# Optimization experiments

Hardware: AMD Instinct MI355X
Metric: run time of the kernel (lower is better)

## Reference

```python
import jax, jax.numpy as jnp
import numpy as np

B, H, T, K = 4, 32, 2048, 64
V = K


def setup_inputs() -> dict:
    key = jax.random.key(0)
    k1, k2, k3, k4, k5 = jax.random.split(key, 5)
    r = jax.random.normal(k1, (B, H, T, K), dtype=jnp.float32)
    k = jax.random.normal(k2, (B, H, T, K), dtype=jnp.float32)
    v = jax.random.normal(k3, (B, H, T, V), dtype=jnp.float32)
    # w is a log-decay; keep it negative so exp(w) in (0,1) and the T-step
    # recurrence is stable (matches real RWKV-6 decay values)
    w = -2.0 * jax.random.uniform(k4, (B, H, T, K), dtype=jnp.float32)
    u = jax.random.normal(k5, (H, K), dtype=jnp.float32)
    initial_state = jnp.zeros((B, H, K, V), dtype=jnp.float32)
    return {"r": r, "k": k, "v": v, "w": w, "u": u, "initial_state": initial_state}


def _rwkv6_scan(r, k, v, w, u, initial_state):
    scale = 1.0
    q = r * scale
    decay = jnp.exp(w)  # [B,H,T,K], matches torch: b_w = exp(w)

    # time-major for scan: [T,B,H,K]
    qT = jnp.moveaxis(q, 2, 0)
    kT = jnp.moveaxis(k, 2, 0)
    vT = jnp.moveaxis(v, 2, 0)
    wT = jnp.moveaxis(decay, 2, 0)

    u_b = u[None, :, :, None]  # [1,H,K,1] broadcast like torch b_u

    def step(h, inp):
        bq, bk, bv, bw = inp  # each [B,H,K] (bv is [B,H,V])
        kv = bk[..., :, None] * bv[..., None, :]          # [B,H,K,V]
        o = jnp.einsum('bhkv,bhk->bhv', h + kv * u_b, bq)  # sum over K
        h = h * bw[..., None] + kv                         # decay-gated update
        return h, o

    final_state, oT = jax.lax.scan(step, initial_state, (qT, kT, vT, wT))
    o = jnp.moveaxis(oT, 0, 2)  # [B,H,T,V]
    return o, final_state


def reference(r, k, v, w, u, initial_state):
    return _rwkv6_scan(r, k, v, w, u, initial_state)
```

## Files before the change

kernel.cpp:

```cpp
#include <hip/hip_runtime.h>
#include <math.h>


#define Bdim 4
#define Hdim 32
#define Tdim 2048
#define Kdim 64
#define Vdim 64
#define NC   32
#define CL   64
#define LP   72

typedef __attribute__((ext_vector_type(8))) short short8;
typedef __attribute__((ext_vector_type(4))) float float4_;

__device__ __forceinline__ short f2bf(float x) {
    unsigned u = __float_as_uint(x);
    unsigned r = (u + 0x7FFFu + ((u >> 16) & 1u)) >> 16;
    return (short)r;
}

#define MFMA(a, b, c) __builtin_amdgcn_mfma_f32_16x16x32_bf16(a, b, c, 0, 0, 0)

__global__ __launch_bounds__(512) void rwkv6_fused(
    const float* __restrict__ rin, const float* __restrict__ kin,
    const float* __restrict__ vin, const float* __restrict__ win,
    const float* __restrict__ uin, const float* __restrict__ init,
    float* __restrict__ oout, float* __restrict__ fin)
{
    __shared__ __attribute__((aligned(16))) short Qh[CL * LP];
    __shared__ __attribute__((aligned(16))) short Kh[CL * LP];
    __shared__ __attribute__((aligned(16))) short Qt[CL * LP];
    __shared__ __attribute__((aligned(16))) short Am[CL * LP];
    __shared__ __attribute__((aligned(16))) short Vt[32 * LP];
    __shared__ __attribute__((aligned(16))) short Ht[32 * LP];
    __shared__ float bsum[8 * 64];
    __shared__ float Dd[CL];

    const int tid  = threadIdx.x;
    const int wv   = tid >> 6;
    const int lane = tid & 63;
    const int quad = lane >> 4, r = lane & 15;

    const int bid = blockIdx.x;
    const int vh  = bid >> 7;
    const int bh  = bid & 127;
    const int h_idx = bh & (Hdim - 1);

    const int m_s = wv >> 2;
    const int n_s = wv & 3;
    const int k_  = 16 * n_s + r;
    const int i_o = wv >> 1;
    const int n_o = wv & 1;

    const float u_ = uin[h_idx * Kdim + lane];

    for (int i = tid; i < CL * LP; i += 512) Am[i] = 0;

    float h[4];
#pragma unroll
    for (int reg = 0; reg < 4; ++reg) {
        const int vloc = 16 * m_s + quad * 4 + reg;
        h[reg] = init[((size_t)bh * Kdim + k_) * Vdim + 32 * vh + vloc];
        Ht[vloc * LP + k_] = f2bf(h[reg]);
    }

    const int tv = tid >> 3;
    const int vl = (tid & 7) * 4;

    float wl[8], ql[8], kl[8];
    float4_ vl4;
    {
        const size_t b0 = (size_t)bh * Tdim * Kdim;
#pragma unroll
        for (int tt = 0; tt < 8; ++tt) {
            const int t = 8 * wv + tt;
            wl[tt] = win[b0 + t * Kdim + lane];
            ql[tt] = rin[b0 + t * Kdim + lane];
            kl[tt] = kin[b0 + t * Kdim + lane];
        }
        vl4 = *(const float4_*)&vin[b0 + tv * Kdim + 32 * vh + vl];
    }

    auto atile = [&](int i, int j) {
        const int trow = 16 * i + r;
        short8 qa0 = *(const short8*)&Qh[trow * LP + quad * 8];
        short8 qa1 = *(const short8*)&Qh[trow * LP + 32 + quad * 8];
        const int srow = 16 * j + r;
        const int sb = (srow >> 3) & 7;
        short8 kb0 = *(const short8*)&Kh[srow * LP + ((quad ^ sb) << 3)];
        short8 kb1 = *(const short8*)&Kh[srow * LP + (((quad + 4) ^ sb) << 3)];
        float4_ acc = {0.f, 0.f, 0.f, 0.f};
        acc = MFMA(qa0, kb0, acc);
        acc = MFMA(qa1, kb1, acc);
#pragma unroll
        for (int reg = 0; reg < 4; ++reg) {
            const int tg = 16 * i + quad * 4 + reg;
            const float val = (tg > srow) ? acc[reg] : ((tg == srow) ? Dd[tg] : 0.f);
            Am[tg * LP + srow] = f2bf(val);
        }
    };

    for (int c = 0; c < NC; ++c) {
        const size_t base = ((size_t)bh * Tdim + (size_t)c * CL) * Kdim;

        float wreg[8];
        float cwl = 0.f;
#pragma unroll
        for (int tt = 0; tt < 8; ++tt) { wreg[tt] = wl[tt]; cwl += wl[tt]; }
        bsum[wv * 64 + lane] = cwl;
#pragma unroll
        for (int i = 0; i < 4; ++i) Vt[(vl + i) * LP + tv] = f2bf(vl4[i]);
        __syncthreads();

        float b[8];
#pragma unroll
        for (int j = 0; j < 8; ++j) b[j] = bsum[j * 64 + lane];
        float pref = 0.f;
#pragma unroll
        for (int j = 0; j < 8; ++j) if (j < wv) pref += b[j];
        const float Cmid = b[0] + b[1] + b[2] + b[3];
        const float eC = __expf(Cmid);
        float cwrun = pref;
#pragma unroll
        for (int tt = 0; tt < 8; ++tt) {
            const int t = 8 * wv + tt;
            const float cwp = cwrun;
            cwrun += wreg[tt];
            const float e1 = __expf(cwp - Cmid);
            Qh[t * LP + lane] = f2bf(ql[tt] * e1);
            Qt[t * LP + lane] = f2bf(ql[tt] * e1 * eC);
            const float e2 = __expf(Cmid - cwrun);
            Kh[t * LP + ((((lane >> 3) ^ ((t >> 3) & 7)) << 3) | (lane & 7))]
                = f2bf(kl[tt] * e2);
            float d3 = ql[tt] * u_ * kl[tt];
#pragma unroll
            for (int off = 32; off > 0; off >>= 1) d3 += __shfl_xor(d3, off);
            if (lane == 0) Dd[t] = d3;
        }
        if (c + 1 < NC) {
            const size_t nb = base + (size_t)CL * Kdim;
#pragma unroll
            for (int tt = 0; tt < 8; ++tt) {
                const int t = 8 * wv + tt;
                wl[tt] = win[nb + t * Kdim + lane];
                ql[tt] = rin[nb + t * Kdim + lane];
                kl[tt] = kin[nb + t * Kdim + lane];
            }
            vl4 = *(const float4_*)&vin[nb + tv * Kdim + 32 * vh + vl];
        }
        __syncthreads();

        {
            int i0, j0;
            if (wv == 0)      { i0 = 0; j0 = 0; }
            else if (wv < 3)  { i0 = 1; j0 = wv - 1; }
            else if (wv < 6)  { i0 = 2; j0 = wv - 3; }
            else              { i0 = 3; j0 = wv - 6; }
            atile(i0, j0);
            if (wv < 2) atile(3, 2 + wv);
        }
        __syncthreads();

        {
            const int trow = 16 * i_o + r;
            short8 aa0 = *(const short8*)&Am[trow * LP + quad * 8];
            short8 aa1 = *(const short8*)&Am[trow * LP + 32 + quad * 8];
            short8 qt0 = *(const short8*)&Qt[trow * LP + quad * 8];
            short8 qt1 = *(const short8*)&Qt[trow * LP + 32 + quad * 8];
            const int vrow = 16 * n_o + r;
            short8 vb0 = *(const short8*)&Vt[vrow * LP + quad * 8];
            short8 vb1 = *(const short8*)&Vt[vrow * LP + 32 + quad * 8];
            short8 hb0 = *(const short8*)&Ht[vrow * LP + quad * 8];
            short8 hb1 = *(const short8*)&Ht[vrow * LP + 32 + quad * 8];
            float4_ o4 = {0.f, 0.f, 0.f, 0.f};
            o4 = MFMA(aa0, vb0, o4);
            o4 = MFMA(aa1, vb1, o4);
            o4 = MFMA(qt0, hb0, o4);
            o4 = MFMA(qt1, hb1, o4);
            float* op = oout + base;
#pragma unroll
            for (int reg = 0; reg < 4; ++reg)
                op[(16 * i_o + quad * 4 + reg) * Vdim + 32 * vh + 16 * n_o + r] = o4[reg];
        }

        float4_ sc = {0.f, 0.f, 0.f, 0.f};
        {
            const int vrow = 16 * m_s + r;
            short8 va0 = *(const short8*)&Vt[vrow * LP + quad * 8];
            short8 va1 = *(const short8*)&Vt[vrow * LP + 32 + quad * 8];
            short8 kc0, kc1;
            const int kb8 = k_ >> 3, k7 = k_ & 7;
#pragma unroll
            for (int j2 = 0; j2 < 8; ++j2) {
                const int s0 = quad * 8 + j2;
                kc0[j2] = Kh[s0 * LP + ((((kb8 ^ (s0 >> 3)) & 7) << 3) | k7)];
                const int s1 = 32 + s0;
                kc1[j2] = Kh[s1 * LP + ((((kb8 ^ (s1 >> 3)) & 7) << 3) | k7)];
            }
            sc = MFMA(va0, kc0, sc);
            sc = MFMA(va1, kc1, sc);
        }
        float totk = 0.f, cmk = 0.f;
#pragma unroll
        for (int j = 0; j < 8; ++j) {
            const float bb = bsum[j * 64 + k_];
            totk += bb;
            if (j < 4) cmk += bb;
        }
        __syncthreads();

        {
            const float eA = __expf(totk);
            const float eS = __expf(totk - cmk);
#pragma unroll
            for (int reg = 0; reg < 4; ++reg) {
                h[reg] = h[reg] * eA + sc[reg] * eS;
                Ht[(16 * m_s + quad * 4 + reg) * LP + k_] = f2bf(h[reg]);
            }
        }
    }

#pragma unroll
    for (int reg = 0; reg < 4; ++reg)
        fin[((size_t)bh * Kdim + k_) * Vdim + 32 * vh + 16 * m_s + quad * 4 + reg] = h[reg];
}

extern "C" void kernel_launch(void* const* d_in, const int* in_sizes, int n_in,
                              void* d_out, int out_size, void* d_ws, size_t ws_size,
                              hipStream_t stream) {
    const float* r    = (const float*)d_in[0];
    const float* k    = (const float*)d_in[1];
    const float* v    = (const float*)d_in[2];
    const float* w    = (const float*)d_in[3];
    const float* u    = (const float*)d_in[4];
    const float* init = (const float*)d_in[5];

    float* o   = (float*)d_out;
    float* fin = o + (size_t)Bdim * Hdim * Tdim * Vdim;

    (void)d_ws; (void)ws_size;
    rwkv6_fused<<<Bdim * Hdim * 2, 512, 0, stream>>>(r, k, v, w, u, init, o, fin);
}
```

Baseline: 311.3 us.

## Add transposed K buffer, swizzled V/H LDS layouts, and lightweight barriers

Adds a transposed copy of the scaled K chunk (KhT) written as packed 16-byte rows, so the state-update MFMA operand becomes two vector LDS reads instead of sixteen scalar gathers. Vt and Ht move to an XOR-swizzled block layout, V is loaded with a different thread mapping and written as packed 4-element stores, and global loads are regrouped by tensor. The __syncthreads calls are replaced by a custom barrier that waits only on LDS counters, so outstanding global prefetches are not drained at each barrier. The cost is extra LDS capacity and stores for the KhT copy, plus reliance on the hand-written barrier being sufficient.

New measurement: 303.5 us. 2.5% less time.

```diff
diff --git a/kernel.cpp b/kernel.cpp
--- a/kernel.cpp
+++ b/kernel.cpp
@@ -12,6 +12,7 @@
 #define LP   72
 
 typedef __attribute__((ext_vector_type(8))) short short8;
+typedef __attribute__((ext_vector_type(4))) short short4_;
 typedef __attribute__((ext_vector_type(4))) float float4_;
 
 __device__ __forceinline__ short f2bf(float x) {
@@ -21,6 +22,13 @@
 }
 
 #define MFMA(a, b, c) __builtin_amdgcn_mfma_f32_16x16x32_bf16(a, b, c, 0, 0, 0)
+
+__device__ __forceinline__ void wg_barrier() {
+    __builtin_amdgcn_sched_barrier(0);
+    asm volatile("s_waitcnt lgkmcnt(0)");
+    __builtin_amdgcn_s_barrier();
+    __builtin_amdgcn_sched_barrier(0);
+}
 
 __global__ __launch_bounds__(512) void rwkv6_fused(
     const float* __restrict__ rin, const float* __restrict__ kin,
@@ -30,6 +38,7 @@
 {
     __shared__ __attribute__((aligned(16))) short Qh[CL * LP];
     __shared__ __attribute__((aligned(16))) short Kh[CL * LP];
+    __shared__ __attribute__((aligned(16))) short KhT[CL * LP];
     __shared__ __attribute__((aligned(16))) short Qt[CL * LP];
     __shared__ __attribute__((aligned(16))) short Am[CL * LP];
     __shared__ __attribute__((aligned(16))) short Vt[32 * LP];
@@ -55,6 +64,14 @@
 
     const float u_ = uin[h_idx * Kdim + lane];
 
+    const int svrow = tid & 31;
+    const int skq   = tid >> 5;
+
+    auto blk_addr = [](const short* buf, int row, int blk) -> const char* {
+        const int phys = blk ^ ((row >> 3) & 3);
+        return (const char*)buf + row * 144 + phys * 16;
+    };
+
     for (int i = tid; i < CL * LP; i += 512) Am[i] = 0;
 
     float h[4];
@@ -62,24 +79,22 @@
     for (int reg = 0; reg < 4; ++reg) {
         const int vloc = 16 * m_s + quad * 4 + reg;
         h[reg] = init[((size_t)bh * Kdim + k_) * Vdim + 32 * vh + vloc];
-        Ht[vloc * LP + k_] = f2bf(h[reg]);
+        const int hb = ((k_ >> 3) ^ ((vloc >> 3) & 3));
+        *(short*)((char*)Ht + vloc * 144 + hb * 16 + (k_ & 7) * 2) = f2bf(h[reg]);
     }
 
-    const int tv = tid >> 3;
-    const int vl = (tid & 7) * 4;
-
-    float wl[8], ql[8], kl[8];
-    float4_ vl4;
+    float wl[8], ql[8], kl[8], vls[4];
     {
         const size_t b0 = (size_t)bh * Tdim * Kdim;
 #pragma unroll
-        for (int tt = 0; tt < 8; ++tt) {
-            const int t = 8 * wv + tt;
-            wl[tt] = win[b0 + t * Kdim + lane];
-            ql[tt] = rin[b0 + t * Kdim + lane];
-            kl[tt] = kin[b0 + t * Kdim + lane];
-        }
-        vl4 = *(const float4_*)&vin[b0 + tv * Kdim + 32 * vh + vl];
+        for (int tt = 0; tt < 8; ++tt) wl[tt] = win[b0 + (8 * wv + tt) * Kdim + lane];
+#pragma unroll
+        for (int i = 0; i < 4; ++i)
+            vls[i] = vin[b0 + (4 * skq + i) * Kdim + 32 * vh + svrow];
+#pragma unroll
+        for (int tt = 0; tt < 8; ++tt) ql[tt] = rin[b0 + (8 * wv + tt) * Kdim + lane];
+#pragma unroll
+        for (int tt = 0; tt < 8; ++tt) kl[tt] = kin[b0 + (8 * wv + tt) * Kdim + lane];
     }
 
     auto atile = [&](int i, int j) {
@@ -109,9 +124,14 @@
 #pragma unroll
         for (int tt = 0; tt < 8; ++tt) { wreg[tt] = wl[tt]; cwl += wl[tt]; }
         bsum[wv * 64 + lane] = cwl;
-#pragma unroll
-        for (int i = 0; i < 4; ++i) Vt[(vl + i) * LP + tv] = f2bf(vl4[i]);
-        __syncthreads();
+        {
+            short4_ pack;
+#pragma unroll
+            for (int i = 0; i < 4; ++i) pack[i] = f2bf(vls[i]);
+            const int vb = ((skq >> 1) ^ ((svrow >> 3) & 3));
+            *(short4_*)((char*)Vt + svrow * 144 + vb * 16 + (skq & 1) * 8) = pack;
+        }
+        wg_barrier();
 
         float b[8];
 #pragma unroll
@@ -122,6 +142,7 @@
         const float Cmid = b[0] + b[1] + b[2] + b[3];
         const float eC = __expf(Cmid);
         float cwrun = pref;
+        short8 khrow;
 #pragma unroll
         for (int tt = 0; tt < 8; ++tt) {
             const int t = 8 * wv + tt;
@@ -131,25 +152,31 @@
             Qh[t * LP + lane] = f2bf(ql[tt] * e1);
             Qt[t * LP + lane] = f2bf(ql[tt] * e1 * eC);
             const float e2 = __expf(Cmid - cwrun);
-            Kh[t * LP + ((((lane >> 3) ^ ((t >> 3) & 7)) << 3) | (lane & 7))]
-                = f2bf(kl[tt] * e2);
+            const short kv = f2bf(kl[tt] * e2);
+            Kh[t * LP + ((((lane >> 3) ^ ((t >> 3) & 7)) << 3) | (lane & 7))] = kv;
+            khrow[tt] = kv;
             float d3 = ql[tt] * u_ * kl[tt];
 #pragma unroll
             for (int off = 32; off > 0; off >>= 1) d3 += __shfl_xor(d3, off);
             if (lane == 0) Dd[t] = d3;
         }
+        {
+            const int kb = (wv ^ ((lane >> 3) & 3));
+            *(short8*)((char*)KhT + lane * 144 + kb * 16) = khrow;
+        }
         if (c + 1 < NC) {
             const size_t nb = base + (size_t)CL * Kdim;
 #pragma unroll
-            for (int tt = 0; tt < 8; ++tt) {
-                const int t = 8 * wv + tt;
-                wl[tt] = win[nb + t * Kdim + lane];
-                ql[tt] = rin[nb + t * Kdim + lane];
-                kl[tt] = kin[nb + t * Kdim + lane];
-            }
-            vl4 = *(const float4_*)&vin[nb + tv * Kdim + 32 * vh + vl];
-        }
-        __syncthreads();
+            for (int tt = 0; tt < 8; ++tt) wl[tt] = win[nb + (8 * wv + tt) * Kdim + lane];
+#pragma unroll
+            for (int i = 0; i < 4; ++i)
+                vls[i] = vin[nb + (4 * skq + i) * Kdim + 32 * vh + svrow];
+#pragma unroll
+            for (int tt = 0; tt < 8; ++tt) ql[tt] = rin[nb + (8 * wv + tt) * Kdim + lane];
+#pragma unroll
+            for (int tt = 0; tt < 8; ++tt) kl[tt] = kin[nb + (8 * wv + tt) * Kdim + lane];
+        }
+        wg_barrier();
 
         {
             int i0, j0;
@@ -160,7 +187,7 @@
             atile(i0, j0);
             if (wv < 2) atile(3, 2 + wv);
         }
-        __syncthreads();
+        wg_barrier();
 
         {
             const int trow = 16 * i_o + r;
@@ -169,10 +196,10 @@
             short8 qt0 = *(const short8*)&Qt[trow * LP + quad * 8];
             short8 qt1 = *(const short8*)&Qt[trow * LP + 32 + quad * 8];
             const int vrow = 16 * n_o + r;
-            short8 vb0 = *(const short8*)&Vt[vrow * LP + quad * 8];
-            short8 vb1 = *(const short8*)&Vt[vrow * LP + 32 + quad * 8];
-            short8 hb0 = *(const short8*)&Ht[vrow * LP + quad * 8];
-            short8 hb1 = *(const short8*)&Ht[vrow * LP + 32 + quad * 8];
+            short8 vb0 = *(const short8*)blk_addr(Vt, vrow, quad);
+            short8 vb1 = *(const short8*)blk_addr(Vt, vrow, quad + 4);
+            short8 hb0 = *(const short8*)blk_addr(Ht, vrow, quad);
+            short8 hb1 = *(const short8*)blk_addr(Ht, vrow, quad + 4);
             float4_ o4 = {0.f, 0.f, 0.f, 0.f};
             o4 = MFMA(aa0, vb0, o4);
             o4 = MFMA(aa1, vb1, o4);
@@ -187,17 +214,10 @@
         float4_ sc = {0.f, 0.f, 0.f, 0.f};
         {
             const int vrow = 16 * m_s + r;
-            short8 va0 = *(const short8*)&Vt[vrow * LP + quad * 8];
-            short8 va1 = *(const short8*)&Vt[vrow * LP + 32 + quad * 8];
-            short8 kc0, kc1;
-            const int kb8 = k_ >> 3, k7 = k_ & 7;
-#pragma unroll
-            for (int j2 = 0; j2 < 8; ++j2) {
-                const int s0 = quad * 8 + j2;
-                kc0[j2] = Kh[s0 * LP + ((((kb8 ^ (s0 >> 3)) & 7) << 3) | k7)];
-                const int s1 = 32 + s0;
-                kc1[j2] = Kh[s1 * LP + ((((kb8 ^ (s1 >> 3)) & 7) << 3) | k7)];
-            }
+            short8 va0 = *(const short8*)blk_addr(Vt, vrow, quad);
+            short8 va1 = *(const short8*)blk_addr(Vt, vrow, quad + 4);
+            short8 kc0 = *(const short8*)blk_addr(KhT, k_, quad);
+            short8 kc1 = *(const short8*)blk_addr(KhT, k_, quad + 4);
             sc = MFMA(va0, kc0, sc);
             sc = MFMA(va1, kc1, sc);
         }
@@ -208,7 +228,7 @@
             totk += bb;
             if (j < 4) cmk += bb;
         }
-        __syncthreads();
+        wg_barrier();
 
         {
             const float eA = __expf(totk);
@@ -216,7 +236,9 @@
 #pragma unroll
             for (int reg = 0; reg < 4; ++reg) {
                 h[reg] = h[reg] * eA + sc[reg] * eS;
-                Ht[(16 * m_s + quad * 4 + reg) * LP + k_] = f2bf(h[reg]);
+                const int vloc = 16 * m_s + quad * 4 + reg;
+                const int hb = ((k_ >> 3) ^ ((vloc >> 3) & 3));
+                *(short*)((char*)Ht + vloc * 144 + hb * 16 + (k_ & 7) * 2) = f2bf(h[reg]);
             }
         }
     }
```
